# Optimization experiments

Measured on AMD Instinct MI355X. Metric: run time of the kernel, lower is better.

## Reference

```python
import jax, jax.numpy as jnp
import numpy as np

MARGIN = 0.5
AP_VALUE = 0.8
AN_VALUE = 0.4
ABS_W = 1.0


def setup_inputs() -> dict:
    key = jax.random.key(0)
    k1, k2 = jax.random.split(key)
    bs, d = 16384, 64
    inputs = jax.random.normal(k1, (bs, d), dtype=jnp.float32)
    target = jax.random.randint(k2, (bs,), 0, 64, dtype=jnp.int64)
    return {"inputs": inputs, "target": target}


def reference(inputs, target):
    # L2-normalize features (normalize_feature=True)
    x = inputs / jnp.linalg.norm(inputs, axis=-1, keepdims=True)

    # cross-entropy on normalized features treated as logits
    logp = jax.nn.log_softmax(x, axis=-1)  # [bs, d]
    loss_ce = -jnp.mean(jnp.take_along_axis(logp, target[:, None], axis=1))

    # cosine-similarity matrix [bs, bs]
    dist = x @ x.T

    is_pos = target[None, :] == target[:, None]
    # hard mining: min similarity among positives, max among negatives (per row)
    dist_ap = jnp.min(jnp.where(is_pos, dist, jnp.inf), axis=1)   # [bs]
    dist_an = jnp.max(jnp.where(is_pos, -jnp.inf, dist), axis=1)  # [bs]

    loss = jnp.mean(jax.nn.relu(MARGIN + dist_ap - dist_an))

    # absolute (angular margin) terms
    abs_ap = jax.nn.relu(AP_VALUE - dist_ap)
    abs_an = jax.nn.relu(dist_an - AN_VALUE)
    loss = (jnp.mean(abs_an) + jnp.mean(abs_ap)) * ABS_W + loss

    return loss + loss_ce
```

## Files before the change

### kernel.cpp

```cpp
#include <hip/hip_runtime.h>


#define N_ROWS 16384
#define N_DIM 64

typedef __attribute__((ext_vector_type(8))) short bf16x8;
typedef __attribute__((ext_vector_type(4))) float f32x4;

__device__ inline unsigned short f2bf(float f) {
  unsigned u = __float_as_uint(f);
  unsigned r = u + 0x7fffu + ((u >> 16) & 1u);
  return (unsigned short)(r >> 16);
}

__device__ inline unsigned enc_key(float f) {
  unsigned u = __float_as_uint(f);
  return (u & 0x80000000u) ? ~u : (u | 0x80000000u);
}
__device__ inline float dec_key(unsigned k) {
  unsigned u = (k & 0x80000000u) ? (k ^ 0x80000000u) : ~k;
  return __uint_as_float(u);
}

__global__ void prep_kernel(const float* __restrict__ x, const int* __restrict__ tgt,
                            unsigned short* __restrict__ xb, float* __restrict__ ce_row) {
  const int row  = blockIdx.x * 4 + (threadIdx.x >> 6);
  const int lane = threadIdx.x & 63;
  float v  = x[row * N_DIM + lane];
  float ss = v * v;
#pragma unroll
  for (int s = 1; s < 64; s <<= 1) ss += __shfl_xor(ss, s, 64);
  float xn = v * rsqrtf(ss);
  xb[row * N_DIM + lane] = f2bf(xn);

  float mx = xn;
#pragma unroll
  for (int s = 1; s < 64; s <<= 1) mx = fmaxf(mx, __shfl_xor(mx, s, 64));
  float e  = __expf(xn - mx);
  float se = e;
#pragma unroll
  for (int s = 1; s < 64; s <<= 1) se += __shfl_xor(se, s, 64);
  float lse = mx + __logf(se);
  int   t   = tgt[row];
  float xt  = __shfl(xn, t, 64);
  if (lane == 0) ce_row[row] = lse - xt;
}

__global__ void mine_kernel(const unsigned short* __restrict__ xb, const int* __restrict__ tgt,
                            unsigned* __restrict__ mp_key, unsigned* __restrict__ mn_key) {
  const int lane    = threadIdx.x & 63;
  const int wv      = threadIdx.x >> 6;
  const int iblk    = blockIdx.x >> 4;
  const int jspl    = blockIdx.x & 15;
  const int rowbase = iblk * 256 + wv * 64;
  const int m = lane & 15, q = lane >> 4;

  bf16x8 a[4][2];
#pragma unroll
  for (int tr = 0; tr < 4; ++tr) {
    const unsigned short* p = xb + (rowbase + tr * 16 + m) * N_DIM + q * 8;
    a[tr][0] = *(const bf16x8*)(p);
    a[tr][1] = *(const bf16x8*)(p + 32);
  }
  int ti[4][4];
#pragma unroll
  for (int tr = 0; tr < 4; ++tr)
#pragma unroll
    for (int r = 0; r < 4; ++r)
      ti[tr][r] = tgt[rowbase + tr * 16 + q * 4 + r];

  float mp[16], mn[16];
#pragma unroll
  for (int k = 0; k < 16; ++k) { mp[k] = __builtin_inff(); mn[k] = -__builtin_inff(); }

  const int jbase = jspl * (N_ROWS / 16);

  const unsigned short* p0 = xb + (jbase + m) * N_DIM + q * 8;
  bf16x8 b0 = *(const bf16x8*)p0;
  bf16x8 b1 = *(const bf16x8*)(p0 + 32);
  int    tj = tgt[jbase + m];

  for (int jc = 0; jc < 64; ++jc) {
    bf16x8 cb0 = b0, cb1 = b1;
    int    ctj = tj;
    if (jc < 63) {
      const int ncol = jbase + (jc + 1) * 16 + m;
      const unsigned short* np = xb + ncol * N_DIM + q * 8;
      b0 = *(const bf16x8*)np;
      b1 = *(const bf16x8*)(np + 32);
      tj = tgt[ncol];
    }
#pragma unroll
    for (int tr = 0; tr < 4; ++tr) {
      f32x4 acc = {0.f, 0.f, 0.f, 0.f};
      acc = __builtin_amdgcn_mfma_f32_16x16x32_bf16(a[tr][0], cb0, acc, 0, 0, 0);
      acc = __builtin_amdgcn_mfma_f32_16x16x32_bf16(a[tr][1], cb1, acc, 0, 0, 0);
#pragma unroll
      for (int r = 0; r < 4; ++r) {
        const bool  pos = (ctj == ti[tr][r]);
        const float d   = acc[r];
        const int   k   = tr * 4 + r;
        mp[k] = fminf(mp[k], pos ? d : __builtin_inff());
        mn[k] = fmaxf(mn[k], pos ? -__builtin_inff() : d);
      }
    }
  }

#pragma unroll
  for (int s = 1; s < 16; s <<= 1) {
#pragma unroll
    for (int k = 0; k < 16; ++k) {
      mp[k] = fminf(mp[k], __shfl_xor(mp[k], s, 64));
      mn[k] = fmaxf(mn[k], __shfl_xor(mn[k], s, 64));
    }
  }
  if (m == 0) {
#pragma unroll
    for (int tr = 0; tr < 4; ++tr)
#pragma unroll
      for (int r = 0; r < 4; ++r) {
        const int row = rowbase + tr * 16 + q * 4 + r;
        atomicMin(&mp_key[row], enc_key(mp[tr * 4 + r]));
        atomicMax(&mn_key[row], enc_key(mn[tr * 4 + r]));
      }
  }
}

__global__ void finalize_kernel(const unsigned* __restrict__ mp_key, const unsigned* __restrict__ mn_key,
                                const float* __restrict__ ce_row, float* __restrict__ out) {
  __shared__ float red[4][16];
  float s1 = 0.f, s2 = 0.f, s3 = 0.f, s4 = 0.f;
  for (int r = threadIdx.x; r < N_ROWS; r += 1024) {
    float ap = dec_key(mp_key[r]);
    float an = dec_key(mn_key[r]);
    s1 += fmaxf(0.5f + ap - an, 0.f);
    s2 += fmaxf(0.8f - ap, 0.f);
    s3 += fmaxf(an - 0.4f, 0.f);
    s4 += ce_row[r];
  }
#pragma unroll
  for (int s = 1; s < 64; s <<= 1) {
    s1 += __shfl_xor(s1, s, 64);
    s2 += __shfl_xor(s2, s, 64);
    s3 += __shfl_xor(s3, s, 64);
    s4 += __shfl_xor(s4, s, 64);
  }
  const int wv = threadIdx.x >> 6;
  if ((threadIdx.x & 63) == 0) {
    red[0][wv] = s1; red[1][wv] = s2; red[2][wv] = s3; red[3][wv] = s4;
  }
  __syncthreads();
  if (threadIdx.x == 0) {
    float t = 0.f;
#pragma unroll
    for (int c = 0; c < 4; ++c) {
      float tc = 0.f;
#pragma unroll
      for (int w = 0; w < 16; ++w) tc += red[c][w];
      t += tc;
    }
    out[0] = t * (1.0f / N_ROWS);
  }
}

extern "C" void kernel_launch(void* const* d_in, const int* in_sizes, int n_in,
                              void* d_out, int out_size, void* d_ws, size_t ws_size,
                              hipStream_t stream) {
  const float* x   = (const float*)d_in[0];
  const int*   tgt = (const int*)d_in[1];
  char* ws = (char*)d_ws;

  unsigned short* xb     = (unsigned short*)ws;
  unsigned*       mp_key = (unsigned*)(ws + (2u << 20));
  unsigned*       mn_key = (unsigned*)(ws + (2u << 20) + (64u << 10));
  float*          ce_row = (float*)(ws + (2u << 20) + (128u << 10));
  float*          out    = (float*)d_out;

  hipMemsetAsync(mp_key, 0xFF, 64u << 10, stream);
  hipMemsetAsync(mn_key, 0x00, 64u << 10, stream);

  prep_kernel<<<N_ROWS / 4, 256, 0, stream>>>(x, tgt, xb, ce_row);
  mine_kernel<<<(N_ROWS / 256) * 16, 256, 0, stream>>>(xb, tgt, mp_key, mn_key);
  finalize_kernel<<<1, 1024, 0, stream>>>(mp_key, mn_key, ce_row, out);
}
```

Baseline: 159.1 us.

## Sort rows by class so mining skips positive checks on non-overlapping tiles

Adds a single-block counting-sort kernel that builds a class-sorted permutation, class offsets, and sorted labels, and moves the key initialisation there in place of the memsets. The prep kernel scatters normalized bf16 rows into sorted order. In the mining kernel each wave knows its row class range, so column tiles outside that range only need a max update with no label compare. The column split also doubles to raise parallelism. The cost is an extra serial launch and a scattered write in prep, and the label compare still runs on tiles that overlap the class range.

```diff
diff --git a/kernel.cpp b/kernel.cpp
--- a/kernel.cpp
+++ b/kernel.cpp
@@ -22,8 +22,42 @@
   return __uint_as_float(u);
 }
 
+__global__ void perm_kernel(const int* __restrict__ tgt, int* __restrict__ perm,
+                            int* __restrict__ ts, int* __restrict__ class_start,
+                            unsigned* __restrict__ mp_key, unsigned* __restrict__ mn_key) {
+  __shared__ int hist[64];
+  __shared__ int start[65];
+  __shared__ int cursor[64];
+  const int tid = threadIdx.x;
+  if (tid < 64) hist[tid] = 0;
+  for (int i = tid; i < N_ROWS; i += 1024) { mp_key[i] = 0xFFFFFFFFu; mn_key[i] = 0u; }
+  __syncthreads();
+  int c[16];
+#pragma unroll
+  for (int k = 0; k < 16; ++k) {
+    c[k] = tgt[tid + k * 1024];
+    atomicAdd(&hist[c[k]], 1);
+  }
+  __syncthreads();
+  if (tid < 64) {
+    int s = 0;
+    for (int j = 0; j < tid; ++j) s += hist[j];
+    start[tid] = s; cursor[tid] = s; class_start[tid] = s;
+    if (tid == 63) { start[64] = s + hist[63]; class_start[64] = s + hist[63]; }
+  }
+  __syncthreads();
+#pragma unroll
+  for (int k = 0; k < 16; ++k) {
+    const int r = tid + k * 1024;
+    const int pos = atomicAdd(&cursor[c[k]], 1);
+    perm[r] = pos;
+    ts[pos] = c[k];
+  }
+}
+
 __global__ void prep_kernel(const float* __restrict__ x, const int* __restrict__ tgt,
-                            unsigned short* __restrict__ xb, float* __restrict__ ce_row) {
+                            const int* __restrict__ perm,
+                            unsigned short* __restrict__ xs, float* __restrict__ ce_row) {
   const int row  = blockIdx.x * 4 + (threadIdx.x >> 6);
   const int lane = threadIdx.x & 63;
   float v  = x[row * N_DIM + lane];
@@ -31,7 +65,7 @@
 #pragma unroll
   for (int s = 1; s < 64; s <<= 1) ss += __shfl_xor(ss, s, 64);
   float xn = v * rsqrtf(ss);
-  xb[row * N_DIM + lane] = f2bf(xn);
+  xs[perm[row] * N_DIM + lane] = f2bf(xn);
 
   float mx = xn;
 #pragma unroll
@@ -46,19 +80,20 @@
   if (lane == 0) ce_row[row] = lse - xt;
 }
 
-__global__ void mine_kernel(const unsigned short* __restrict__ xb, const int* __restrict__ tgt,
+__global__ void mine_kernel(const unsigned short* __restrict__ xs, const int* __restrict__ ts,
+                            const int* __restrict__ class_start,
                             unsigned* __restrict__ mp_key, unsigned* __restrict__ mn_key) {
   const int lane    = threadIdx.x & 63;
   const int wv      = threadIdx.x >> 6;
-  const int iblk    = blockIdx.x >> 4;
-  const int jspl    = blockIdx.x & 15;
+  const int iblk    = blockIdx.x >> 5;
+  const int jspl    = blockIdx.x & 31;
   const int rowbase = iblk * 256 + wv * 64;
   const int m = lane & 15, q = lane >> 4;
 
   bf16x8 a[4][2];
 #pragma unroll
   for (int tr = 0; tr < 4; ++tr) {
-    const unsigned short* p = xb + (rowbase + tr * 16 + m) * N_DIM + q * 8;
+    const unsigned short* p = xs + (rowbase + tr * 16 + m) * N_DIM + q * 8;
     a[tr][0] = *(const bf16x8*)(p);
     a[tr][1] = *(const bf16x8*)(p + 32);
   }
@@ -67,41 +102,57 @@
   for (int tr = 0; tr < 4; ++tr)
 #pragma unroll
     for (int r = 0; r < 4; ++r)
-      ti[tr][r] = tgt[rowbase + tr * 16 + q * 4 + r];
+      ti[tr][r] = ts[rowbase + tr * 16 + q * 4 + r];
+
+  const int cmin = ts[rowbase];
+  const int cmax = ts[rowbase + 63];
+  const int lo   = class_start[cmin];
+  const int hi   = class_start[cmax + 1];
 
   float mp[16], mn[16];
 #pragma unroll
   for (int k = 0; k < 16; ++k) { mp[k] = __builtin_inff(); mn[k] = -__builtin_inff(); }
 
-  const int jbase = jspl * (N_ROWS / 16);
-
-  const unsigned short* p0 = xb + (jbase + m) * N_DIM + q * 8;
+  const int jbase = jspl * 512;
+
+  const unsigned short* p0 = xs + (jbase + m) * N_DIM + q * 8;
   bf16x8 b0 = *(const bf16x8*)p0;
   bf16x8 b1 = *(const bf16x8*)(p0 + 32);
-  int    tj = tgt[jbase + m];
-
-  for (int jc = 0; jc < 64; ++jc) {
+
+  for (int jc = 0; jc < 32; ++jc) {
     bf16x8 cb0 = b0, cb1 = b1;
-    int    ctj = tj;
-    if (jc < 63) {
-      const int ncol = jbase + (jc + 1) * 16 + m;
-      const unsigned short* np = xb + ncol * N_DIM + q * 8;
+    const int jb = jbase + jc * 16;
+    if (jc < 31) {
+      const unsigned short* np = xs + (jb + 16 + m) * N_DIM + q * 8;
       b0 = *(const bf16x8*)np;
       b1 = *(const bf16x8*)(np + 32);
-      tj = tgt[ncol];
-    }
-#pragma unroll
-    for (int tr = 0; tr < 4; ++tr) {
-      f32x4 acc = {0.f, 0.f, 0.f, 0.f};
-      acc = __builtin_amdgcn_mfma_f32_16x16x32_bf16(a[tr][0], cb0, acc, 0, 0, 0);
-      acc = __builtin_amdgcn_mfma_f32_16x16x32_bf16(a[tr][1], cb1, acc, 0, 0, 0);
-#pragma unroll
-      for (int r = 0; r < 4; ++r) {
-        const bool  pos = (ctj == ti[tr][r]);
-        const float d   = acc[r];
-        const int   k   = tr * 4 + r;
-        mp[k] = fminf(mp[k], pos ? d : __builtin_inff());
-        mn[k] = fmaxf(mn[k], pos ? -__builtin_inff() : d);
+    }
+    const bool slow = (jb < hi) && (jb + 16 > lo);
+    if (slow) {
+      const int ctj = ts[jb + m];
+#pragma unroll
+      for (int tr = 0; tr < 4; ++tr) {
+        f32x4 acc = {0.f, 0.f, 0.f, 0.f};
+        acc = __builtin_amdgcn_mfma_f32_16x16x32_bf16(a[tr][0], cb0, acc, 0, 0, 0);
+        acc = __builtin_amdgcn_mfma_f32_16x16x32_bf16(a[tr][1], cb1, acc, 0, 0, 0);
+#pragma unroll
+        for (int r = 0; r < 4; ++r) {
+          const bool  pos = (ctj == ti[tr][r]);
+          const float d   = acc[r];
+          const int   k   = tr * 4 + r;
+          mp[k] = fminf(mp[k], pos ? d : __builtin_inff());
+          mn[k] = fmaxf(mn[k], pos ? -__builtin_inff() : d);
+        }
+      }
+    } else {
+#pragma unroll
+      for (int tr = 0; tr < 4; ++tr) {
+        f32x4 acc = {0.f, 0.f, 0.f, 0.f};
+        acc = __builtin_amdgcn_mfma_f32_16x16x32_bf16(a[tr][0], cb0, acc, 0, 0, 0);
+        acc = __builtin_amdgcn_mfma_f32_16x16x32_bf16(a[tr][1], cb1, acc, 0, 0, 0);
+#pragma unroll
+        for (int r = 0; r < 4; ++r)
+          mn[tr * 4 + r] = fmaxf(mn[tr * 4 + r], acc[r]);
       }
     }
   }
@@ -170,16 +221,17 @@
   const int*   tgt = (const int*)d_in[1];
   char* ws = (char*)d_ws;
 
-  unsigned short* xb     = (unsigned short*)ws;
+  unsigned short* xs     = (unsigned short*)ws;
   unsigned*       mp_key = (unsigned*)(ws + (2u << 20));
   unsigned*       mn_key = (unsigned*)(ws + (2u << 20) + (64u << 10));
   float*          ce_row = (float*)(ws + (2u << 20) + (128u << 10));
+  int*            perm   = (int*)(ws + (2u << 20) + (192u << 10));
+  int*            ts     = (int*)(ws + (2u << 20) + (256u << 10));
+  int*            cstart = (int*)(ws + (2u << 20) + (320u << 10));
   float*          out    = (float*)d_out;
 
-  hipMemsetAsync(mp_key, 0xFF, 64u << 10, stream);
-  hipMemsetAsync(mn_key, 0x00, 64u << 10, stream);
-
-  prep_kernel<<<N_ROWS / 4, 256, 0, stream>>>(x, tgt, xb, ce_row);
-  mine_kernel<<<(N_ROWS / 256) * 16, 256, 0, stream>>>(xb, tgt, mp_key, mn_key);
+  perm_kernel<<<1, 1024, 0, stream>>>(tgt, perm, ts, cstart, mp_key, mn_key);
+  prep_kernel<<<N_ROWS / 4, 256, 0, stream>>>(x, tgt, perm, xs, ce_row);
+  mine_kernel<<<64 * 32, 256, 0, stream>>>(xs, ts, cstart, mp_key, mn_key);
   finalize_kernel<<<1, 1024, 0, stream>>>(mp_key, mn_key, ce_row, out);
 }
```

After: 167.8 us. 1.06x slower.
